# Performance work log

Measured on AMD Instinct MI355X. Metric: run time of the kernel, lower is better.

Reference implementation:

```python
import jax, jax.numpy as jnp
import numpy as np

B, DIN, DOUT = 4096, 4096, 4096

def setup_inputs() -> dict:
    key = jax.random.key(0)
    k1, k2, k3 = jax.random.split(key, 3)
    x = jax.random.normal(k1, (B, DIN), dtype=jnp.float32)
    W = jax.random.normal(k2, (DOUT, DIN), dtype=jnp.float32) * 0.01
    alpha = jnp.ones((DOUT, DIN), dtype=jnp.float32) * 0.01
    eta = jnp.asarray(0.1, dtype=jnp.float32)
    bias = jnp.zeros((DOUT,), dtype=jnp.float32)
    return {"x": x, "W": W, "alpha": alpha, "eta": eta, "bias": bias}

def reference(x, W, alpha, eta, bias):
    # y_slow = x @ W.T + b                          (B, DOUT)
    y_slow = jnp.einsum('bi,oi->bo', x, W) + bias
    # x_norm = x / (||x|| + 1e-8)
    x_norm = x / (jnp.linalg.norm(x, axis=-1, keepdims=True) + 1e-8)
    y_pre = jnp.tanh(y_slow)
    # plastic_i = eta * y_pre_i * sum_j sigmoid(alpha)_ij * x_norm_j * x_j
    # (algebraic rewrite of bmm over per-sample outer-product trace; same math)
    s = jnp.einsum('bi,oi->bo', x_norm * x, jax.nn.sigmoid(alpha))  # (B, DOUT)
    plastic = eta * y_pre * s
    return y_slow + plastic
```

## Files before the change

### kernel.cpp

```cpp
#include <hip/hip_runtime.h>
#include <hip/hip_bf16.h>
#include <math.h>


typedef __attribute__((ext_vector_type(4))) float floatx4;
typedef __attribute__((ext_vector_type(8))) short shortx8;

#define MAT_N 4096
#define MAT_ELEMS ((size_t)MAT_N * MAT_N)

__device__ __forceinline__ unsigned short f2bf(float f) {
    unsigned int u = __float_as_uint(f);
    unsigned int r = (u + 0x7fffu + ((u >> 16) & 1u)) >> 16;
    return (unsigned short)r;
}

__device__ __forceinline__ void gload_lds16(const unsigned short* gptr, unsigned short* lptr) {
    __builtin_amdgcn_global_load_lds(
        (const __attribute__((address_space(1))) unsigned int*)gptr,
        (__attribute__((address_space(3))) unsigned int*)lptr,
        16, 0, 0);
}

__global__ __launch_bounds__(256) void conv_all_kernel(const float* __restrict__ x,
                                                       const float* __restrict__ W,
                                                       const float* __restrict__ alpha,
                                                       unsigned short* __restrict__ xb,
                                                       unsigned short* __restrict__ pb,
                                                       unsigned short* __restrict__ wb,
                                                       unsigned short* __restrict__ ab) {
    if (blockIdx.x < MAT_N) {
        const int row = blockIdx.x;
        const float4* xr = (const float4*)(x + (size_t)row * MAT_N);
        float4 v[4];
        float s = 0.f;
#pragma unroll
        for (int i = 0; i < 4; i++) {
            v[i] = xr[threadIdx.x + i * 256];
            s += v[i].x * v[i].x + v[i].y * v[i].y + v[i].z * v[i].z + v[i].w * v[i].w;
        }
        for (int off = 32; off > 0; off >>= 1) s += __shfl_down(s, off, 64);
        __shared__ float red[4];
        if ((threadIdx.x & 63) == 0) red[threadIdx.x >> 6] = s;
        __syncthreads();
        const float inv = 1.0f / (sqrtf(red[0] + red[1] + red[2] + red[3]) + 1e-8f);
        unsigned short* xrow = xb + (size_t)row * MAT_N;
        unsigned short* prow = pb + (size_t)row * MAT_N;
#pragma unroll
        for (int i = 0; i < 4; i++) {
            float e[4] = {v[i].x, v[i].y, v[i].z, v[i].w};
            ushort4 xo, po;
            xo.x = f2bf(e[0]); xo.y = f2bf(e[1]); xo.z = f2bf(e[2]); xo.w = f2bf(e[3]);
            po.x = f2bf(e[0] * e[0] * inv); po.y = f2bf(e[1] * e[1] * inv);
            po.z = f2bf(e[2] * e[2] * inv); po.w = f2bf(e[3] * e[3] * inv);
            *(ushort4*)(xrow + (threadIdx.x + i * 256) * 4) = xo;
            *(ushort4*)(prow + (threadIdx.x + i * 256) * 4) = po;
        }
    } else {
        size_t base = ((size_t)(blockIdx.x - MAT_N) * 256 + threadIdx.x) * 8;
        const float4* wp = (const float4*)(W + base);
        const float4* ap = (const float4*)(alpha + base);
        float4 w0 = wp[0], w1 = wp[1], a0 = ap[0], a1 = ap[1];
        float wv[8] = {w0.x, w0.y, w0.z, w0.w, w1.x, w1.y, w1.z, w1.w};
        float av[8] = {a0.x, a0.y, a0.z, a0.w, a1.x, a1.y, a1.z, a1.w};
        shortx8 wo, ao;
#pragma unroll
        for (int j = 0; j < 8; j++) {
            wo[j] = (short)f2bf(wv[j]);
            ao[j] = (short)f2bf(1.0f / (1.0f + __expf(-av[j])));
        }
        *(shortx8*)(wb + base) = wo;
        *(shortx8*)(ab + base) = ao;
    }
}

__global__ __launch_bounds__(512, 4) void fused_gemm_kernel(
    const unsigned short* __restrict__ X,
    const unsigned short* __restrict__ Wb,
    const unsigned short* __restrict__ P,
    const unsigned short* __restrict__ Ab,
    const float* __restrict__ bias,
    const float* __restrict__ eta_p,
    float* __restrict__ out) {
    constexpr int K = MAT_N;
    constexpr int N = MAT_N;
    constexpr int BK = 64;
    __shared__ __align__(16) unsigned short sX[128 * BK];
    __shared__ __align__(16) unsigned short sW[128 * BK];
    __shared__ __align__(16) unsigned short sP[128 * BK];
    __shared__ __align__(16) unsigned short sA[128 * BK];

    const int tid = threadIdx.x;
    const int row0 = blockIdx.y * 128;
    const int col0 = blockIdx.x * 128;
    const int lane = tid & 63;
    const int wave = tid >> 6;
    const int wm = (wave >> 1) * 32;
    const int wn = (wave & 1) * 64;
    const int quad = lane >> 4;
    const int l16 = lane & 15;

    floatx4 accY[2][4], accS[2][4];
#pragma unroll
    for (int i = 0; i < 2; i++)
#pragma unroll
        for (int j = 0; j < 4; j++) {
            accY[i][j] = (floatx4){0.f, 0.f, 0.f, 0.f};
            accS[i][j] = (floatx4){0.f, 0.f, 0.f, 0.f};
        }

    const int row_s = tid >> 3;
    const int kc_g  = (tid & 7) ^ (row_s & 7);
    const size_t arow = (size_t)(row0 + row_s) * K + kc_g * 8;
    const size_t brow = (size_t)(col0 + row_s) * K + kc_g * 8;

    for (int k0 = 0; k0 < K; k0 += BK) {
#pragma unroll
        for (int i = 0; i < 2; i++) {
            const size_t go = (size_t)i * 64 * K + k0;
            const int lo = i * 4096 + tid * 8;
            gload_lds16(X + arow + go, sX + lo);
            gload_lds16(Wb + brow + go, sW + lo);
            gload_lds16(P + arow + go, sP + lo);
            gload_lds16(Ab + brow + go, sA + lo);
        }
        __syncthreads();

#pragma unroll
        for (int s = 0; s < 2; s++) {
            const int kcp = ((s * 4 + quad) ^ (l16 & 7)) * 8;
            {
                shortx8 af[2], bfr[4];
#pragma unroll
                for (int i = 0; i < 2; i++)
                    af[i] = *(const shortx8*)(sX + (wm + i * 16 + l16) * BK + kcp);
#pragma unroll
                for (int j = 0; j < 4; j++)
                    bfr[j] = *(const shortx8*)(sW + (wn + j * 16 + l16) * BK + kcp);
#pragma unroll
                for (int i = 0; i < 2; i++)
#pragma unroll
                    for (int j = 0; j < 4; j++)
                        accY[i][j] = __builtin_amdgcn_mfma_f32_16x16x32_bf16(af[i], bfr[j], accY[i][j], 0, 0, 0);
            }
            {
                shortx8 af[2], bfr[4];
#pragma unroll
                for (int i = 0; i < 2; i++)
                    af[i] = *(const shortx8*)(sP + (wm + i * 16 + l16) * BK + kcp);
#pragma unroll
                for (int j = 0; j < 4; j++)
                    bfr[j] = *(const shortx8*)(sA + (wn + j * 16 + l16) * BK + kcp);
#pragma unroll
                for (int i = 0; i < 2; i++)
#pragma unroll
                    for (int j = 0; j < 4; j++)
                        accS[i][j] = __builtin_amdgcn_mfma_f32_16x16x32_bf16(af[i], bfr[j], accS[i][j], 0, 0, 0);
            }
        }
        __syncthreads();
    }

    const float eta = *eta_p;
#pragma unroll
    for (int i = 0; i < 2; i++) {
#pragma unroll
        for (int j = 0; j < 4; j++) {
#pragma unroll
            for (int r = 0; r < 4; r++) {
                int grow = row0 + wm + i * 16 + quad * 4 + r;
                int gcol = col0 + wn + j * 16 + l16;
                float y = accY[i][j][r] + bias[gcol];
                float s = accS[i][j][r];
                out[(size_t)grow * N + gcol] = y + eta * tanhf(y) * s;
            }
        }
    }
}

extern "C" void kernel_launch(void* const* d_in, const int* in_sizes, int n_in,
                              void* d_out, int out_size, void* d_ws, size_t ws_size,
                              hipStream_t stream) {
    const float* x     = (const float*)d_in[0];
    const float* W     = (const float*)d_in[1];
    const float* alpha = (const float*)d_in[2];
    const float* eta   = (const float*)d_in[3];
    const float* bias  = (const float*)d_in[4];
    float* out = (float*)d_out;

    unsigned short* xb = (unsigned short*)d_ws;
    unsigned short* pb = xb + MAT_ELEMS;
    unsigned short* wb = pb + MAT_ELEMS;
    unsigned short* ab = wb + MAT_ELEMS;

    conv_all_kernel<<<MAT_N + MAT_ELEMS / (8 * 256), 256, 0, stream>>>(x, W, alpha, xb, pb, wb, ab);

    dim3 grid(MAT_N / 128, MAT_N / 128);
    fused_gemm_kernel<<<grid, 512, 0, stream>>>(xb, wb, pb, ab, bias, eta, out);
}
```

Baseline: 513.4 us.

## Run plastic-term GEMM in FP8 and defer row normalization to epilogue

The second GEMM (x² times sigmoid(alpha)) now uses FP8 operands and the fp8 MFMA instead of bf16. This halves the LDS and global traffic for those operands. Row norms are accumulated with atomics in a separate conversion kernel and applied in the GEMM epilogue rather than folded into P. The preprocessing is split into two elementwise kernels plus a memset. FP8 precision on the plastic term risks accuracy, and squared x values are stored unnormalized in FP8, which narrows their usable range.

```diff
diff --git a/kernel.cpp b/kernel.cpp
--- a/kernel.cpp
+++ b/kernel.cpp
@@ -15,80 +15,82 @@
     return (unsigned short)r;
 }
 
-__device__ __forceinline__ void gload_lds16(const unsigned short* gptr, unsigned short* lptr) {
+__device__ __forceinline__ void gload_lds16(const void* gptr, void* lptr) {
     __builtin_amdgcn_global_load_lds(
         (const __attribute__((address_space(1))) unsigned int*)gptr,
         (__attribute__((address_space(3))) unsigned int*)lptr,
         16, 0, 0);
 }
 
-__global__ __launch_bounds__(256) void conv_all_kernel(const float* __restrict__ x,
-                                                       const float* __restrict__ W,
-                                                       const float* __restrict__ alpha,
-                                                       unsigned short* __restrict__ xb,
-                                                       unsigned short* __restrict__ pb,
-                                                       unsigned short* __restrict__ wb,
-                                                       unsigned short* __restrict__ ab) {
-    if (blockIdx.x < MAT_N) {
-        const int row = blockIdx.x;
-        const float4* xr = (const float4*)(x + (size_t)row * MAT_N);
-        float4 v[4];
-        float s = 0.f;
-#pragma unroll
-        for (int i = 0; i < 4; i++) {
-            v[i] = xr[threadIdx.x + i * 256];
-            s += v[i].x * v[i].x + v[i].y * v[i].y + v[i].z * v[i].z + v[i].w * v[i].w;
-        }
-        for (int off = 32; off > 0; off >>= 1) s += __shfl_down(s, off, 64);
-        __shared__ float red[4];
-        if ((threadIdx.x & 63) == 0) red[threadIdx.x >> 6] = s;
-        __syncthreads();
-        const float inv = 1.0f / (sqrtf(red[0] + red[1] + red[2] + red[3]) + 1e-8f);
-        unsigned short* xrow = xb + (size_t)row * MAT_N;
-        unsigned short* prow = pb + (size_t)row * MAT_N;
-#pragma unroll
-        for (int i = 0; i < 4; i++) {
-            float e[4] = {v[i].x, v[i].y, v[i].z, v[i].w};
-            ushort4 xo, po;
-            xo.x = f2bf(e[0]); xo.y = f2bf(e[1]); xo.z = f2bf(e[2]); xo.w = f2bf(e[3]);
-            po.x = f2bf(e[0] * e[0] * inv); po.y = f2bf(e[1] * e[1] * inv);
-            po.z = f2bf(e[2] * e[2] * inv); po.w = f2bf(e[3] * e[3] * inv);
-            *(ushort4*)(xrow + (threadIdx.x + i * 256) * 4) = xo;
-            *(ushort4*)(prow + (threadIdx.x + i * 256) * 4) = po;
-        }
-    } else {
-        size_t base = ((size_t)(blockIdx.x - MAT_N) * 256 + threadIdx.x) * 8;
-        const float4* wp = (const float4*)(W + base);
-        const float4* ap = (const float4*)(alpha + base);
-        float4 w0 = wp[0], w1 = wp[1], a0 = ap[0], a1 = ap[1];
-        float wv[8] = {w0.x, w0.y, w0.z, w0.w, w1.x, w1.y, w1.z, w1.w};
-        float av[8] = {a0.x, a0.y, a0.z, a0.w, a1.x, a1.y, a1.z, a1.w};
-        shortx8 wo, ao;
-#pragma unroll
-        for (int j = 0; j < 8; j++) {
-            wo[j] = (short)f2bf(wv[j]);
-            ao[j] = (short)f2bf(1.0f / (1.0f + __expf(-av[j])));
-        }
-        *(shortx8*)(wb + base) = wo;
-        *(shortx8*)(ab + base) = ao;
-    }
+__global__ __launch_bounds__(512) void convx_kernel(const float* __restrict__ x,
+                                                    unsigned short* __restrict__ xb,
+                                                    unsigned char* __restrict__ p8,
+                                                    float* __restrict__ sumsq) {
+    size_t base = ((size_t)blockIdx.x * 512 + threadIdx.x) * 8;
+    const float4* xp = (const float4*)(x + base);
+    float4 a = xp[0], b = xp[1];
+    float v[8] = {a.x, a.y, a.z, a.w, b.x, b.y, b.z, b.w};
+    shortx8 xo;
+    float sq[8];
+    float s = 0.f;
+#pragma unroll
+    for (int j = 0; j < 8; j++) {
+        xo[j] = (short)f2bf(v[j]);
+        sq[j] = v[j] * v[j];
+        s += sq[j];
+    }
+    *(shortx8*)(xb + base) = xo;
+    int p0 = __builtin_amdgcn_cvt_pk_fp8_f32(sq[0], sq[1], 0, false);
+    p0 = __builtin_amdgcn_cvt_pk_fp8_f32(sq[2], sq[3], p0, true);
+    int p1 = __builtin_amdgcn_cvt_pk_fp8_f32(sq[4], sq[5], 0, false);
+    p1 = __builtin_amdgcn_cvt_pk_fp8_f32(sq[6], sq[7], p1, true);
+    int2 pv = {p0, p1};
+    *(int2*)(p8 + base) = pv;
+    for (int off = 32; off > 0; off >>= 1) s += __shfl_down(s, off, 64);
+    if ((threadIdx.x & 63) == 0) atomicAdd(&sumsq[base >> 12], s);
+}
+
+__global__ __launch_bounds__(512) void convwa_kernel(const float* __restrict__ W,
+                                                     const float* __restrict__ alpha,
+                                                     unsigned short* __restrict__ wb,
+                                                     unsigned char* __restrict__ a8) {
+    size_t base = ((size_t)blockIdx.x * 512 + threadIdx.x) * 8;
+    const float4* wp = (const float4*)(W + base);
+    const float4* ap = (const float4*)(alpha + base);
+    float4 w0 = wp[0], w1 = wp[1], a0 = ap[0], a1 = ap[1];
+    float wv[8] = {w0.x, w0.y, w0.z, w0.w, w1.x, w1.y, w1.z, w1.w};
+    float av[8] = {a0.x, a0.y, a0.z, a0.w, a1.x, a1.y, a1.z, a1.w};
+    shortx8 wo;
+    float sg[8];
+#pragma unroll
+    for (int j = 0; j < 8; j++) {
+        wo[j] = (short)f2bf(wv[j]);
+        sg[j] = 1.0f / (1.0f + __expf(-av[j]));
+    }
+    *(shortx8*)(wb + base) = wo;
+    int p0 = __builtin_amdgcn_cvt_pk_fp8_f32(sg[0], sg[1], 0, false);
+    p0 = __builtin_amdgcn_cvt_pk_fp8_f32(sg[2], sg[3], p0, true);
+    int p1 = __builtin_amdgcn_cvt_pk_fp8_f32(sg[4], sg[5], 0, false);
+    p1 = __builtin_amdgcn_cvt_pk_fp8_f32(sg[6], sg[7], p1, true);
+    int2 pv = {p0, p1};
+    *(int2*)(a8 + base) = pv;
 }
 
 __global__ __launch_bounds__(512, 4) void fused_gemm_kernel(
     const unsigned short* __restrict__ X,
     const unsigned short* __restrict__ Wb,
-    const unsigned short* __restrict__ P,
-    const unsigned short* __restrict__ Ab,
+    const unsigned char* __restrict__ P8,
+    const unsigned char* __restrict__ A8,
     const float* __restrict__ bias,
     const float* __restrict__ eta_p,
+    const float* __restrict__ sumsq,
     float* __restrict__ out) {
     constexpr int K = MAT_N;
     constexpr int N = MAT_N;
-    constexpr int BK = 64;
-    __shared__ __align__(16) unsigned short sX[128 * BK];
-    __shared__ __align__(16) unsigned short sW[128 * BK];
-    __shared__ __align__(16) unsigned short sP[128 * BK];
-    __shared__ __align__(16) unsigned short sA[128 * BK];
+    __shared__ __align__(16) unsigned short sX[128 * 64];
+    __shared__ __align__(16) unsigned short sW[128 * 64];
+    __shared__ __align__(16) unsigned char  sP[128 * 64];
+    __shared__ __align__(16) unsigned char  sA[128 * 64];
 
     const int tid = threadIdx.x;
     const int row0 = blockIdx.y * 128;
@@ -113,30 +115,35 @@
     const int kc_g  = (tid & 7) ^ (row_s & 7);
     const size_t arow = (size_t)(row0 + row_s) * K + kc_g * 8;
     const size_t brow = (size_t)(col0 + row_s) * K + kc_g * 8;
-
-    for (int k0 = 0; k0 < K; k0 += BK) {
+    const int r8 = tid >> 2;
+    const int slot8 = (2 * (tid & 3)) ^ (r8 & 6);
+    const size_t prow = (size_t)(row0 + r8) * K + slot8 * 8;
+    const size_t qrow = (size_t)(col0 + r8) * K + slot8 * 8;
+
+    for (int k0 = 0; k0 < K; k0 += 64) {
 #pragma unroll
         for (int i = 0; i < 2; i++) {
             const size_t go = (size_t)i * 64 * K + k0;
             const int lo = i * 4096 + tid * 8;
             gload_lds16(X + arow + go, sX + lo);
             gload_lds16(Wb + brow + go, sW + lo);
-            gload_lds16(P + arow + go, sP + lo);
-            gload_lds16(Ab + brow + go, sA + lo);
-        }
+        }
+        gload_lds16(P8 + prow + k0, sP + tid * 16);
+        gload_lds16(A8 + qrow + k0, sA + tid * 16);
         __syncthreads();
 
 #pragma unroll
         for (int s = 0; s < 2; s++) {
             const int kcp = ((s * 4 + quad) ^ (l16 & 7)) * 8;
+            const int lsp = ((s * 4 + quad) ^ (l16 & 6)) * 8;
             {
                 shortx8 af[2], bfr[4];
 #pragma unroll
                 for (int i = 0; i < 2; i++)
-                    af[i] = *(const shortx8*)(sX + (wm + i * 16 + l16) * BK + kcp);
+                    af[i] = *(const shortx8*)(sX + (wm + i * 16 + l16) * 64 + kcp);
 #pragma unroll
                 for (int j = 0; j < 4; j++)
-                    bfr[j] = *(const shortx8*)(sW + (wn + j * 16 + l16) * BK + kcp);
+                    bfr[j] = *(const shortx8*)(sW + (wn + j * 16 + l16) * 64 + kcp);
 #pragma unroll
                 for (int i = 0; i < 2; i++)
 #pragma unroll
@@ -144,18 +151,18 @@
                         accY[i][j] = __builtin_amdgcn_mfma_f32_16x16x32_bf16(af[i], bfr[j], accY[i][j], 0, 0, 0);
             }
             {
-                shortx8 af[2], bfr[4];
-#pragma unroll
-                for (int i = 0; i < 2; i++)
-                    af[i] = *(const shortx8*)(sP + (wm + i * 16 + l16) * BK + kcp);
+                long ap[2], bp[4];
+#pragma unroll
+                for (int i = 0; i < 2; i++)
+                    ap[i] = *(const long*)(sP + (wm + i * 16 + l16) * 64 + lsp);
 #pragma unroll
                 for (int j = 0; j < 4; j++)
-                    bfr[j] = *(const shortx8*)(sA + (wn + j * 16 + l16) * BK + kcp);
+                    bp[j] = *(const long*)(sA + (wn + j * 16 + l16) * 64 + lsp);
 #pragma unroll
                 for (int i = 0; i < 2; i++)
 #pragma unroll
                     for (int j = 0; j < 4; j++)
-                        accS[i][j] = __builtin_amdgcn_mfma_f32_16x16x32_bf16(af[i], bfr[j], accS[i][j], 0, 0, 0);
+                        accS[i][j] = __builtin_amdgcn_mfma_f32_16x16x32_fp8_fp8(ap[i], bp[j], accS[i][j], 0, 0, 0);
             }
         }
         __syncthreads();
@@ -165,13 +172,14 @@
 #pragma unroll
     for (int i = 0; i < 2; i++) {
 #pragma unroll
-        for (int j = 0; j < 4; j++) {
-#pragma unroll
-            for (int r = 0; r < 4; r++) {
-                int grow = row0 + wm + i * 16 + quad * 4 + r;
-                int gcol = col0 + wn + j * 16 + l16;
+        for (int r = 0; r < 4; r++) {
+            const int grow = row0 + wm + i * 16 + quad * 4 + r;
+            const float invn = 1.0f / (sqrtf(sumsq[grow]) + 1e-8f);
+#pragma unroll
+            for (int j = 0; j < 4; j++) {
+                const int gcol = col0 + wn + j * 16 + l16;
                 float y = accY[i][j][r] + bias[gcol];
-                float s = accS[i][j][r];
+                float s = accS[i][j][r] * invn;
                 out[(size_t)grow * N + gcol] = y + eta * tanhf(y) * s;
             }
         }
@@ -188,13 +196,17 @@
     const float* bias  = (const float*)d_in[4];
     float* out = (float*)d_out;
 
-    unsigned short* xb = (unsigned short*)d_ws;
-    unsigned short* pb = xb + MAT_ELEMS;
-    unsigned short* wb = pb + MAT_ELEMS;
-    unsigned short* ab = wb + MAT_ELEMS;
-
-    conv_all_kernel<<<MAT_N + MAT_ELEMS / (8 * 256), 256, 0, stream>>>(x, W, alpha, xb, pb, wb, ab);
+    char* ws = (char*)d_ws;
+    float* sumsq = (float*)ws;
+    unsigned short* xb = (unsigned short*)(ws + 16384);
+    unsigned short* wb = xb + MAT_ELEMS;
+    unsigned char*  p8 = (unsigned char*)(wb + MAT_ELEMS);
+    unsigned char*  a8 = p8 + MAT_ELEMS;
+
+    hipMemsetAsync(sumsq, 0, MAT_N * sizeof(float), stream);
+    convx_kernel<<<MAT_ELEMS / (8 * 512), 512, 0, stream>>>(x, xb, p8, sumsq);
+    convwa_kernel<<<MAT_ELEMS / (8 * 512), 512, 0, stream>>>(W, alpha, wb, a8);
 
     dim3 grid(MAT_N / 128, MAT_N / 128);
-    fused_gemm_kernel<<<grid, 512, 0, stream>>>(xb, wb, pb, ab, bias, eta, out);
-}
+    fused_gemm_kernel<<<grid, 512, 0, stream>>>(xb, wb, p8, a8, bias, eta, sumsq, out);
+}
```

Result: faster. 466.3 us (-9.2%).
